# Kernel optimization log

Measured on AMD Instinct MI355X. Metric: run time of the kernel, lower is better.

The kernel has to match this reference:

```python
import jax, jax.numpy as jnp
import numpy as np

E, B, D, H, Z = 8, 16384, 512, 512, 64   # experts, batch, input_dim, hidden, latent
NHID = 2                                 # num_mlp_layers - 1 hidden-to-hidden layers


def setup_inputs() -> dict:
    key = jax.random.key(0)
    ks = jax.random.split(key, 12)

    def w(k, shape, fan_in):
        return (jax.random.normal(k, shape, jnp.float32) / np.sqrt(fan_in)).astype(jnp.float32)

    return {
        "x": jax.random.normal(ks[0], (B, D), jnp.float32),
        "eps": jax.random.normal(ks[1], (B, Z), jnp.float32),
        # stacked per-expert parameters (leading axis E)
        "enc_in_w": w(ks[2], (E, D, H), D), "enc_in_b": jnp.zeros((E, H), jnp.float32),
        "enc_hid_w": w(ks[3], (E, NHID, H, H), H), "enc_hid_b": jnp.zeros((E, NHID, H), jnp.float32),
        "mu_w": w(ks[4], (E, H, Z), H), "mu_b": jnp.zeros((E, Z), jnp.float32),
        "lv_w": w(ks[5], (E, H, Z), H), "lv_b": jnp.zeros((E, Z), jnp.float32),
        "dec_in_w": w(ks[6], (E, Z, H), Z), "dec_in_b": jnp.zeros((E, H), jnp.float32),
        "dec_hid_w": w(ks[7], (E, NHID, H, H), H), "dec_hid_b": jnp.zeros((E, NHID, H), jnp.float32),
        "dec_out_w": w(ks[8], (E, H, D), H), "dec_out_b": jnp.zeros((E, D), jnp.float32),
    }


def _moe_forward(x, eps, enc_in_w, enc_in_b, enc_hid_w, enc_hid_b,
                 mu_w, mu_b, lv_w, lv_b,
                 dec_in_w, dec_in_b, dec_hid_w, dec_hid_b, dec_out_w, dec_out_b):
    # ---- every expert tries the problem (dense, all experts over full batch) ----
    h = jax.nn.relu(jnp.einsum('bd,edh->ebh', x, enc_in_w) + enc_in_b[:, None, :])
    for i in range(NHID):
        h = jax.nn.relu(jnp.einsum('ebh,ehk->ebk', h, enc_hid_w[:, i]) + enc_hid_b[:, i, None, :])
    mu = jnp.einsum('ebh,ehz->ebz', h, mu_w) + mu_b[:, None, :]          # [E,B,Z]
    logvar = jnp.einsum('ebh,ehz->ebz', h, lv_w) + lv_b[:, None, :]       # [E,B,Z]
    z = mu + jnp.exp(0.5 * logvar) * eps[None, :, :]                      # reparameterize
    g = jax.nn.relu(jnp.einsum('ebz,ezh->ebh', z, dec_in_w) + dec_in_b[:, None, :])
    for i in range(NHID):
        g = jax.nn.relu(jnp.einsum('ebh,ehk->ebk', g, dec_hid_w[:, i]) + dec_hid_b[:, i, None, :])
    xhat = jnp.einsum('ebh,ehd->ebd', g, dec_out_w) + dec_out_b[:, None, :]  # [E,B,D]

    # ---- per-sample recon loss, pick best expert (torch.min over experts) ----
    recon = jnp.mean((xhat - x[None, :, :]) ** 2, axis=-1)                # [E,B]
    expert_idx = jnp.argmin(recon, axis=0)                                # [B]

    # ---- sparse_others: single fused gather instead of python loop ----
    bi = jnp.arange(x.shape[0])
    return mu[expert_idx, bi], logvar[expert_idx, bi], xhat[expert_idx, bi]


def reference(x, eps, enc_in_w, enc_in_b, enc_hid_w, enc_hid_b,
              mu_w, mu_b, lv_w, lv_b,
              dec_in_w, dec_in_b, dec_hid_w, dec_hid_b, dec_out_w, dec_out_b):
    return _moe_forward(x, eps, enc_in_w, enc_in_b, enc_hid_w, enc_hid_b,
                        mu_w, mu_b, lv_w, lv_b,
                        dec_in_w, dec_in_b, dec_hid_w, dec_hid_b, dec_out_w, dec_out_b)
```

## Files before the change

### kernel.cpp

```cpp
#include <hip/hip_runtime.h>
#include <cstdint>

#define Eexp 8
#define Bb   16384
#define Dd   512
#define Hh   512
#define Zz   64

typedef _Float16 f16x8 __attribute__((ext_vector_type(8)));
typedef float    f32x4 __attribute__((ext_vector_type(4)));

#define OFF_ENCIN  0
#define OFF_HID0   524288
#define OFF_HID1   1048576
#define OFF_HEADS  1572864
#define OFF_DECIN  1703936
#define OFF_DHID0  1769472
#define OFF_DHID1  2293760
#define OFF_DECOUT 2818048
#define PEREXP     3342336
#define WT_TOTAL   (8 * (size_t)PEREXP)

#define GLL16(g, l) __builtin_amdgcn_global_load_lds( \
    (const __attribute__((address_space(1))) void*)(g), \
    (__attribute__((address_space(3))) void*)(l), 16, 0, 0)

template<bool TR>
__global__ __launch_bounds__(256)
void fmsplit(const float* __restrict__ src, _Float16* __restrict__ dst,
             int KTOT, int inner, long sStride, long dStride)
{
    __shared__ float t[64][65];
    const int e  = blockIdx.z;
    const int o0 = blockIdx.x * 64;
    const int k0 = blockIdx.y * 64;
    const float* S = src + (size_t)e * sStride;
    _Float16*    D = dst + (size_t)e * dStride;
    const int tid = threadIdx.x;
    const int rr = tid >> 4, c4 = (tid & 15) * 4;
    #pragma unroll
    for (int p = 0; p < 4; ++p) {
        const int r = rr + p * 16;
        const float4 v = *reinterpret_cast<const float4*>(
            S + (size_t)(TR ? (k0 + r) : (o0 + r)) * inner + (TR ? o0 : k0) + c4);
        t[r][c4 + 0] = v.x; t[r][c4 + 1] = v.y;
        t[r][c4 + 2] = v.z; t[r][c4 + 3] = v.w;
    }
    __syncthreads();
    const int lane = tid & 63, wid = tid >> 6;
    const int KB = KTOT >> 5;
    #pragma unroll
    for (int p = 0; p < 2; ++p) {
        const int g  = wid * 2 + p;
        const int ot = g >> 1, kb = g & 1;
        const int rI = ot * 16 + (lane & 15);
        const int kI = kb * 32 + (lane >> 4) * 8;
        f16x8 hv, lv;
        #pragma unroll
        for (int j = 0; j < 8; ++j) {
            const float v = TR ? t[kI + j][rI] : t[rI][kI + j];
            const _Float16 h = (_Float16)v;
            hv[j] = h; lv[j] = (_Float16)(v - (float)h);
        }
        const size_t base = ((size_t)((o0 >> 4) + ot) * KB + (k0 >> 5) + kb) * 1024;
        *reinterpret_cast<f16x8*>(D + base + lane * 8)       = hv;
        *reinterpret_cast<f16x8*>(D + base + 512 + lane * 8) = lv;
    }
}

template<int KA>
__global__ __launch_bounds__(256, 2)
void gemm_mid(const _Float16* __restrict__ Afm, const _Float16* __restrict__ Wfm,
              const float* __restrict__ bias0, _Float16* __restrict__ Cfm)
{
    constexpr int KB  = KA / 32;
    constexpr int NT  = KB;
    constexpr int ACH = 16;
    constexpr int NCH = 32;
    constexpr int GPW = 8;
    __shared__ __align__(16) _Float16 lds[2 * NCH * 512];

    const int bid = blockIdx.x;
    const int bx = (bid & 7) * 16 + (bid >> 5);
    const int by = (bid >> 3) & 3;

    const int lane = threadIdx.x & 63, wid = threadIdx.x >> 6;
    const int wr = wid >> 1, wc = wid & 1;
    const int row0 = bx * 128;
    const int col0 = by * 128;

    const _Float16* src[GPW];
    #pragma unroll
    for (int p = 0; p < GPW; ++p) {
        const int q = wid * GPW + p;
        if (q < ACH)
            src[p] = Afm + (size_t)((row0 >> 4) + (q >> 1)) * KB * 1024
                         + (q & 1) * 512 + lane * 8;
        else {
            const int qq = q - ACH;
            src[p] = Wfm + (size_t)((col0 >> 4) + (qq >> 1)) * KB * 1024
                         + (qq & 1) * 512 + lane * 8;
        }
    }

    f32x4 acc[4][4];
    #pragma unroll
    for (int i = 0; i < 4; ++i)
        #pragma unroll
        for (int j = 0; j < 4; ++j) acc[i][j] = {0.f, 0.f, 0.f, 0.f};

#define STAGE(buf)                                                           \
    { _Pragma("unroll")                                                      \
      for (int p = 0; p < GPW; ++p) {                                        \
          GLL16(src[p], lds + (buf) * (NCH * 512) + (wid * GPW + p) * 512);  \
          src[p] += 1024;                                                    \
      } }

    STAGE(0)
    if (NT > 1) STAGE(1)

    for (int t = 0; t < NT; ++t) {
        if (t + 1 < NT) { asm volatile("s_waitcnt vmcnt(%0)" :: "i"(GPW) : "memory"); }
        else            { asm volatile("s_waitcnt vmcnt(0)" ::: "memory"); }
        __builtin_amdgcn_s_barrier();
        asm volatile("" ::: "memory");

        const _Float16* B0 = lds + (t & 1) * (NCH * 512);
        f16x8 ah[4], al[4], wh[4], wl[4];
        #pragma unroll
        for (int mf = 0; mf < 4; ++mf) {
            const int q = (wr * 4 + mf) * 2;
            ah[mf] = *reinterpret_cast<const f16x8*>(B0 + q * 512 + lane * 8);
            al[mf] = *reinterpret_cast<const f16x8*>(B0 + q * 512 + 512 + lane * 8);
        }
        #pragma unroll
        for (int nf = 0; nf < 4; ++nf) {
            const int q = ACH + (wc * 4 + nf) * 2;
            wh[nf] = *reinterpret_cast<const f16x8*>(B0 + q * 512 + lane * 8);
            wl[nf] = *reinterpret_cast<const f16x8*>(B0 + q * 512 + 512 + lane * 8);
        }
        __builtin_amdgcn_s_setprio(1);
        #pragma unroll
        for (int mf = 0; mf < 4; ++mf)
            #pragma unroll
            for (int nf = 0; nf < 4; ++nf) {
                acc[mf][nf] = __builtin_amdgcn_mfma_f32_16x16x32_f16(
                    ah[mf], wh[nf], acc[mf][nf], 0, 0, 0);
                acc[mf][nf] = __builtin_amdgcn_mfma_f32_16x16x32_f16(
                    ah[mf], wl[nf], acc[mf][nf], 0, 0, 0);
                acc[mf][nf] = __builtin_amdgcn_mfma_f32_16x16x32_f16(
                    al[mf], wh[nf], acc[mf][nf], 0, 0, 0);
            }
        __builtin_amdgcn_s_setprio(0);
        asm volatile("" ::: "memory");
        __builtin_amdgcn_s_barrier();
        asm volatile("" ::: "memory");
        if (t + 2 < NT) STAGE(t & 1)
    }
#undef STAGE

    uint32_t* sb = reinterpret_cast<uint32_t*>(&lds[0]);
    #pragma unroll
    for (int ph = 0; ph < 2; ++ph) {
        if (wc == ph) {
            #pragma unroll
            for (int nf = 0; nf < 4; ++nf) {
                const int c_l = nf * 16 + (lane & 15);
                const float bv = bias0[col0 + ph * 64 + c_l];
                #pragma unroll
                for (int mf = 0; mf < 4; ++mf)
                    #pragma unroll
                    for (int j = 0; j < 4; ++j) {
                        const int r_l = wr * 64 + mf * 16 + (lane >> 4) * 4 + j;
                        const float v = fmaxf(acc[mf][nf][j] + bv, 0.f);
                        const _Float16 h = (_Float16)v;
                        const _Float16 lo = (_Float16)(v - (float)h);
                        const uint32_t pk =
                            (uint32_t)__builtin_bit_cast(uint16_t, h) |
                            ((uint32_t)__builtin_bit_cast(uint16_t, lo) << 16);
                        sb[r_l * 64 + (((c_l >> 2) ^ (r_l & 15)) << 2) + (c_l & 3)] = pk;
                    }
            }
        }
        __syncthreads();
        {
            #pragma unroll
            for (int i = 0; i < 4; ++i) {
                const int q = wid * 4 + i;
                const int T_l = q >> 1, kb_l = q & 1;
                const int r_l = T_l * 16 + (lane & 15);
                const int cb  = kb_l * 32 + (lane >> 4) * 8;
                uint32_t u[8];
                #pragma unroll
                for (int jb = 0; jb < 2; ++jb) {
                    const int chunk = ((cb >> 2) + jb) ^ (r_l & 15);
                    const uint32_t* pp = &sb[r_l * 64 + chunk * 4];
                    u[jb*4+0] = pp[0]; u[jb*4+1] = pp[1];
                    u[jb*4+2] = pp[2]; u[jb*4+3] = pp[3];
                }
                f16x8 hv, lvv;
                #pragma unroll
                for (int j = 0; j < 8; ++j) {
                    hv[j]  = __builtin_bit_cast(_Float16, (uint16_t)(u[j] & 0xffff));
                    lvv[j] = __builtin_bit_cast(_Float16, (uint16_t)(u[j] >> 16));
                }
                const size_t base =
                    ((size_t)((row0 >> 4) + T_l) * 16 +
                     ((col0 + ph * 64) >> 5) + kb_l) * 1024;
                *reinterpret_cast<f16x8*>(Cfm + base + lane * 8)       = hv;
                *reinterpret_cast<f16x8*>(Cfm + base + 512 + lane * 8) = lvv;
            }
        }
        __syncthreads();
    }
}

__global__ __launch_bounds__(256, 2)
void heads_z(const _Float16* __restrict__ Afm, const _Float16* __restrict__ Wfm,
             const float* __restrict__ mu_b, const float* __restrict__ lv_b,
             const float* __restrict__ eps,
             float* __restrict__ mu_e, float* __restrict__ lv_e,
             _Float16* __restrict__ zfm)
{
    constexpr int KB = 16, NT = 16, ACH = 8, NCH = 24, GPW = 6;
    __shared__ __align__(16) _Float16 lds[2 * NCH * 512];

    const int bid = blockIdx.x;
    const int bx = (bid & 7) * 32 + (bid >> 3);
    const int lane = threadIdx.x & 63, wid = threadIdx.x >> 6;
    const int wr = wid >> 1, wc = wid & 1;
    const int row0 = bx * 64;

    const _Float16* src[GPW];
    #pragma unroll
    for (int p = 0; p < GPW; ++p) {
        const int q = wid * GPW + p;
        if (q < ACH)
            src[p] = Afm + (size_t)((row0 >> 4) + (q >> 1)) * KB * 1024
                         + (q & 1) * 512 + lane * 8;
        else {
            const int qq = q - ACH;
            src[p] = Wfm + (size_t)(qq >> 1) * KB * 1024 + (qq & 1) * 512 + lane * 8;
        }
    }

    f32x4 acc[2][4];
    #pragma unroll
    for (int i = 0; i < 2; ++i)
        #pragma unroll
        for (int j = 0; j < 4; ++j) acc[i][j] = {0.f, 0.f, 0.f, 0.f};

#define STAGE(buf)                                                           \
    { _Pragma("unroll")                                                      \
      for (int p = 0; p < GPW; ++p) {                                        \
          GLL16(src[p], lds + (buf) * (NCH * 512) + (wid * GPW + p) * 512);  \
          src[p] += 1024;                                                    \
      } }

    STAGE(0)
    STAGE(1)

    for (int t = 0; t < NT; ++t) {
        if (t + 1 < NT) { asm volatile("s_waitcnt vmcnt(%0)" :: "i"(GPW) : "memory"); }
        else            { asm volatile("s_waitcnt vmcnt(0)" ::: "memory"); }
        __builtin_amdgcn_s_barrier();
        asm volatile("" ::: "memory");

        const _Float16* B0 = lds + (t & 1) * (NCH * 512);
        f16x8 ah[2], al[2], wh[4], wl[4];
        #pragma unroll
        for (int mf = 0; mf < 2; ++mf) {
            const int q = (wr * 2 + mf) * 2;
            ah[mf] = *reinterpret_cast<const f16x8*>(B0 + q * 512 + lane * 8);
            al[mf] = *reinterpret_cast<const f16x8*>(B0 + q * 512 + 512 + lane * 8);
        }
        #pragma unroll
        for (int nf = 0; nf < 4; ++nf) {
            const int q = ACH + (wc * 4 + nf) * 2;
            wh[nf] = *reinterpret_cast<const f16x8*>(B0 + q * 512 + lane * 8);
            wl[nf] = *reinterpret_cast<const f16x8*>(B0 + q * 512 + 512 + lane * 8);
        }
        __builtin_amdgcn_s_setprio(1);
        #pragma unroll
        for (int mf = 0; mf < 2; ++mf)
            #pragma unroll
            for (int nf = 0; nf < 4; ++nf) {
                acc[mf][nf] = __builtin_amdgcn_mfma_f32_16x16x32_f16(
                    ah[mf], wh[nf], acc[mf][nf], 0, 0, 0);
                acc[mf][nf] = __builtin_amdgcn_mfma_f32_16x16x32_f16(
                    ah[mf], wl[nf], acc[mf][nf], 0, 0, 0);
                acc[mf][nf] = __builtin_amdgcn_mfma_f32_16x16x32_f16(
                    al[mf], wh[nf], acc[mf][nf], 0, 0, 0);
            }
        __builtin_amdgcn_s_setprio(0);
        asm volatile("" ::: "memory");
        __builtin_amdgcn_s_barrier();
        asm volatile("" ::: "memory");
        if (t + 2 < NT) STAGE(t & 1)
    }
#undef STAGE

    float* mulv = reinterpret_cast<float*>(&lds[0]);
    #pragma unroll
    for (int nf = 0; nf < 4; ++nf) {
        const int c_h = wc * 64 + nf * 16 + (lane & 15);
        const float bv = (c_h < 64) ? mu_b[c_h] : lv_b[c_h - 64];
        #pragma unroll
        for (int mf = 0; mf < 2; ++mf)
            #pragma unroll
            for (int j = 0; j < 4; ++j) {
                const int r_l = wr * 32 + mf * 16 + (lane >> 4) * 4 + j;
                mulv[r_l * 128 + c_h] = acc[mf][nf][j] + bv;
            }
    }
    __syncthreads();
    const int tid = threadIdx.x;
    #pragma unroll
    for (int k = 0; k < 16; ++k) {
        const int id  = tid + k * 256;
        const int r_l = id >> 6, c = id & 63;
        const float m = mulv[r_l * 128 + c];
        const float l = mulv[r_l * 128 + 64 + c];
        const size_t go = (size_t)(row0 + r_l) * 64 + c;
        const float ev = eps[go];
        const float z  = m + expf(0.5f * l) * ev;
        mu_e[go] = m; lv_e[go] = l;
        const _Float16 h  = (_Float16)z;
        const _Float16 lo = (_Float16)(z - (float)h);
        const size_t base = ((size_t)((row0 + r_l) >> 4) * 2 + (c >> 5)) * 1024
                            + ((r_l & 15) + ((c >> 3) & 3) * 16) * 8 + (c & 7);
        zfm[base]       = h;
        zfm[base + 512] = lo;
    }
}

__global__ __launch_bounds__(512, 2)
void dec_out_fused(const _Float16* __restrict__ Afm, const _Float16* __restrict__ Wfm,
                   const float* __restrict__ bias,
                   const float* __restrict__ Xin,
                   const float* __restrict__ mu_e, const float* __restrict__ lv_e,
                   float* __restrict__ best,
                   float* __restrict__ out_mu, float* __restrict__ out_lv,
                   float* __restrict__ out_xh, int isFirst)
{
    constexpr int KB = 16, NT = 16, ACH = 8, NCH = 72, GPW = 9;
    __shared__ __align__(16) _Float16 lds[2 * NCH * 512];

    const int bid = blockIdx.x;
    const int bx = (bid & 7) * 32 + (bid >> 3);
    const int lane = threadIdx.x & 63, wid = threadIdx.x >> 6;
    const int row0 = bx * 64;
    const int colW = wid * 64;

    const _Float16* src[GPW];
    #pragma unroll
    for (int p = 0; p < GPW; ++p) {
        const int q = wid * GPW + p;
        if (q < ACH)
            src[p] = Afm + (size_t)((row0 >> 4) + (q >> 1)) * KB * 1024
                         + (q & 1) * 512 + lane * 8;
        else {
            const int qq = q - ACH;
            src[p] = Wfm + (size_t)(qq >> 1) * KB * 1024 + (qq & 1) * 512 + lane * 8;
        }
    }

    f32x4 acc[4][4];
    #pragma unroll
    for (int i = 0; i < 4; ++i)
        #pragma unroll
        for (int j = 0; j < 4; ++j) acc[i][j] = {0.f, 0.f, 0.f, 0.f};

#define STAGE(buf)                                                           \
    { _Pragma("unroll")                                                      \
      for (int p = 0; p < GPW; ++p) {                                        \
          GLL16(src[p], lds + (buf) * (NCH * 512) + (wid * GPW + p) * 512);  \
          src[p] += 1024;                                                    \
      } }

    STAGE(0)
    STAGE(1)

    for (int t = 0; t < NT; ++t) {
        if (t + 1 < NT) { asm volatile("s_waitcnt vmcnt(%0)" :: "i"(GPW) : "memory"); }
        else            { asm volatile("s_waitcnt vmcnt(0)" ::: "memory"); }
        __builtin_amdgcn_s_barrier();
        asm volatile("" ::: "memory");

        const _Float16* B0 = lds + (t & 1) * (NCH * 512);
        f16x8 ah[4], al[4], wh[4], wl[4];
        #pragma unroll
        for (int mf = 0; mf < 4; ++mf) {
            const int q = mf * 2;
            ah[mf] = *reinterpret_cast<const f16x8*>(B0 + q * 512 + lane * 8);
            al[mf] = *reinterpret_cast<const f16x8*>(B0 + q * 512 + 512 + lane * 8);
        }
        #pragma unroll
        for (int nf = 0; nf < 4; ++nf) {
            const int q = ACH + (wid * 4 + nf) * 2;
            wh[nf] = *reinterpret_cast<const f16x8*>(B0 + q * 512 + lane * 8);
            wl[nf] = *reinterpret_cast<const f16x8*>(B0 + q * 512 + 512 + lane * 8);
        }
        __builtin_amdgcn_s_setprio(1);
        #pragma unroll
        for (int mf = 0; mf < 4; ++mf)
            #pragma unroll
            for (int nf = 0; nf < 4; ++nf) {
                acc[mf][nf] = __builtin_amdgcn_mfma_f32_16x16x32_f16(
                    ah[mf], wh[nf], acc[mf][nf], 0, 0, 0);
                acc[mf][nf] = __builtin_amdgcn_mfma_f32_16x16x32_f16(
                    ah[mf], wl[nf], acc[mf][nf], 0, 0, 0);
                acc[mf][nf] = __builtin_amdgcn_mfma_f32_16x16x32_f16(
                    al[mf], wh[nf], acc[mf][nf], 0, 0, 0);
            }
        __builtin_amdgcn_s_setprio(0);
        asm volatile("" ::: "memory");
        __builtin_amdgcn_s_barrier();
        asm volatile("" ::: "memory");
        if (t + 2 < NT) STAGE(t & 1)
    }
#undef STAGE

    float*    recP = reinterpret_cast<float*>(&lds[0]);
    int*      winf = reinterpret_cast<int*>(recP + 8 * 64);

    float rsum[4][4];
    #pragma unroll
    for (int mf = 0; mf < 4; ++mf)
        #pragma unroll
        for (int j = 0; j < 4; ++j) rsum[mf][j] = 0.f;
    float bv[4];
    #pragma unroll
    for (int nf = 0; nf < 4; ++nf) bv[nf] = bias[colW + nf * 16 + (lane & 15)];
    #pragma unroll
    for (int nf = 0; nf < 4; ++nf) {
        const int col = colW + nf * 16 + (lane & 15);
        #pragma unroll
        for (int mf = 0; mf < 4; ++mf)
            #pragma unroll
            for (int j = 0; j < 4; ++j) {
                const int r_l = mf * 16 + (lane >> 4) * 4 + j;
                const float v = acc[mf][nf][j] + bv[nf];
                const float d = v - Xin[(size_t)(row0 + r_l) * 512 + col];
                rsum[mf][j] += d * d;
            }
    }
    #pragma unroll
    for (int mf = 0; mf < 4; ++mf)
        #pragma unroll
        for (int j = 0; j < 4; ++j) {
            float s = rsum[mf][j];
            s += __shfl_xor(s, 1); s += __shfl_xor(s, 2);
            s += __shfl_xor(s, 4); s += __shfl_xor(s, 8);
            if ((lane & 15) == 0)
                recP[wid * 64 + mf * 16 + (lane >> 4) * 4 + j] = s;
        }
    __syncthreads();
    if (wid == 0) {
        float r = 0.f;
        #pragma unroll
        for (int w = 0; w < 8; ++w) r += recP[w * 64 + lane];
        const int grow = row0 + lane;
        const bool w = isFirst || (r < best[grow]);
        if (w) best[grow] = r;
        winf[lane] = w ? 1 : 0;
    }
    __syncthreads();
    #pragma unroll
    for (int mf = 0; mf < 4; ++mf)
        #pragma unroll
        for (int j = 0; j < 4; ++j) {
            const int r_l = mf * 16 + (lane >> 4) * 4 + j;
            if (winf[r_l]) {
                #pragma unroll
                for (int nf = 0; nf < 4; ++nf) {
                    const int col = colW + nf * 16 + (lane & 15);
                    out_xh[(size_t)(row0 + r_l) * 512 + col] = acc[mf][nf][j] + bv[nf];
                }
            }
        }
    if (wid == 0) {
        for (int r = 0; r < 64; ++r)
            if (winf[r]) {
                const size_t o = (size_t)(row0 + r) * 64 + lane;
                out_mu[o] = mu_e[o];
            }
    } else if (wid == 1) {
        for (int r = 0; r < 64; ++r)
            if (winf[r]) {
                const size_t o = (size_t)(row0 + r) * 64 + lane;
                out_lv[o] = lv_e[o];
            }
    }
}

extern "C" void kernel_launch(void* const* d_in, const int* in_sizes, int n_in,
                              void* d_out, int out_size, void* d_ws, size_t ws_size,
                              hipStream_t stream)
{
    const float* x         = (const float*)d_in[0];
    const float* eps       = (const float*)d_in[1];
    const float* enc_in_w  = (const float*)d_in[2];
    const float* enc_in_b  = (const float*)d_in[3];
    const float* enc_hid_w = (const float*)d_in[4];
    const float* enc_hid_b = (const float*)d_in[5];
    const float* mu_w      = (const float*)d_in[6];
    const float* mu_b      = (const float*)d_in[7];
    const float* lv_w      = (const float*)d_in[8];
    const float* lv_b      = (const float*)d_in[9];
    const float* dec_in_w  = (const float*)d_in[10];
    const float* dec_in_b  = (const float*)d_in[11];
    const float* dec_hid_w = (const float*)d_in[12];
    const float* dec_hid_b = (const float*)d_in[13];
    const float* dec_out_w = (const float*)d_in[14];
    const float* dec_out_b = (const float*)d_in[15];

    const size_t FM = (size_t)Bb * 512 * 2;
    const size_t BZ = (size_t)Bb * 64;

    _Float16* wt  = (_Float16*)d_ws;
    _Float16* xfm = wt + WT_TOTAL;
    _Float16* afm = xfm + FM;
    _Float16* bfm = afm + FM;
    _Float16* zfm = bfm + FM;
    float* fbase  = (float*)(zfm + (size_t)Bb * 64 * 2);
    float* mu_e   = fbase;
    float* lv_e   = mu_e + BZ;
    float* best   = lv_e + BZ;

    float* out_mu = (float*)d_out;
    float* out_lv = out_mu + (size_t)Bb * Zz;
    float* out_xh = out_lv + (size_t)Bb * Zz;

    const dim3 blk(256);

    fmsplit<true ><<<dim3(8, 8, 8), blk, 0, stream>>>(enc_in_w,           wt + OFF_ENCIN,  512, 512, 262144, PEREXP);
    fmsplit<true ><<<dim3(8, 8, 8), blk, 0, stream>>>(enc_hid_w,          wt + OFF_HID0,   512, 512, 524288, PEREXP);
    fmsplit<true ><<<dim3(8, 8, 8), blk, 0, stream>>>(enc_hid_w + 262144, wt + OFF_HID1,   512, 512, 524288, PEREXP);
    fmsplit<true ><<<dim3(1, 8, 8), blk, 0, stream>>>(mu_w,               wt + OFF_HEADS,  512,  64,  32768, PEREXP);
    fmsplit<true ><<<dim3(1, 8, 8), blk, 0, stream>>>(lv_w,        wt + OFF_HEADS + 65536, 512,  64,  32768, PEREXP);
    fmsplit<true ><<<dim3(8, 1, 8), blk, 0, stream>>>(dec_in_w,           wt + OFF_DECIN,   64, 512,  32768, PEREXP);
    fmsplit<true ><<<dim3(8, 8, 8), blk, 0, stream>>>(dec_hid_w,          wt + OFF_DHID0,  512, 512, 524288, PEREXP);
    fmsplit<true ><<<dim3(8, 8, 8), blk, 0, stream>>>(dec_hid_w + 262144, wt + OFF_DHID1,  512, 512, 524288, PEREXP);
    fmsplit<true ><<<dim3(8, 8, 8), blk, 0, stream>>>(dec_out_w,          wt + OFF_DECOUT, 512, 512, 262144, PEREXP);
    fmsplit<false><<<dim3(256, 8, 1), blk, 0, stream>>>(x,                xfm,             512, 512, 0, 0);

    const dim3 g512(512), g256(256), blk512(512);

    for (int e = 0; e < Eexp; ++e) {
        const _Float16* we = wt + (size_t)e * PEREXP;
        gemm_mid<512><<<g512, blk, 0, stream>>>(
            xfm, we + OFF_ENCIN, enc_in_b + (size_t)e * Hh, afm);
        gemm_mid<512><<<g512, blk, 0, stream>>>(
            afm, we + OFF_HID0, enc_hid_b + ((size_t)e * 2 + 0) * Hh, bfm);
        gemm_mid<512><<<g512, blk, 0, stream>>>(
            bfm, we + OFF_HID1, enc_hid_b + ((size_t)e * 2 + 1) * Hh, afm);
        heads_z<<<g256, blk, 0, stream>>>(
            afm, we + OFF_HEADS, mu_b + (size_t)e * Zz, lv_b + (size_t)e * Zz,
            eps, mu_e, lv_e, zfm);
        gemm_mid< 64><<<g512, blk, 0, stream>>>(
            zfm, we + OFF_DECIN, dec_in_b + (size_t)e * Hh, bfm);
        gemm_mid<512><<<g512, blk, 0, stream>>>(
            bfm, we + OFF_DHID0, dec_hid_b + ((size_t)e * 2 + 0) * Hh, afm);
        gemm_mid<512><<<g512, blk, 0, stream>>>(
            afm, we + OFF_DHID1, dec_hid_b + ((size_t)e * 2 + 1) * Hh, bfm);
        dec_out_fused<<<g256, blk512, 0, stream>>>(
            bfm, we + OFF_DECOUT, dec_out_b + (size_t)e * Dd,
            x, mu_e, lv_e, best, out_mu, out_lv, out_xh, e == 0 ? 1 : 0);
    }
}
```

Baseline: 1.757 ms.

## Load decoder-output weights straight to registers and shrink LDS staging to activations

The dec_out_fused kernel now stages only the activation tiles through LDS with async global-to-LDS loads. Each wave reads its own weight fragments directly from global memory into registers every k-step, instead of staging all 72 chunks through LDS. LDS usage drops sharply and launch bounds change to one block per SIMD hint, which allows more registers. The mu/logvar winner copy is also spread across all 8 waves instead of 2. The risks are exposed global-load latency on the weight reads, since they are issued just before the wait, and a fragile hand-tuned vmcnt accounting.

```diff
diff --git a/kernel.cpp b/kernel.cpp
--- a/kernel.cpp
+++ b/kernel.cpp
@@ -334,7 +334,7 @@
     }
 }
 
-__global__ __launch_bounds__(512, 2)
+__global__ __launch_bounds__(512, 1)
 void dec_out_fused(const _Float16* __restrict__ Afm, const _Float16* __restrict__ Wfm,
                    const float* __restrict__ bias,
                    const float* __restrict__ Xin,
@@ -343,8 +343,8 @@
                    float* __restrict__ out_mu, float* __restrict__ out_lv,
                    float* __restrict__ out_xh, int isFirst)
 {
-    constexpr int KB = 16, NT = 16, ACH = 8, NCH = 72, GPW = 9;
-    __shared__ __align__(16) _Float16 lds[2 * NCH * 512];
+    constexpr int KB = 16, NT = 16;
+    __shared__ __align__(16) _Float16 lds[2 * 8 * 512];
 
     const int bid = blockIdx.x;
     const int bx = (bid & 7) * 32 + (bid >> 3);
@@ -352,18 +352,13 @@
     const int row0 = bx * 64;
     const int colW = wid * 64;
 
-    const _Float16* src[GPW];
-    #pragma unroll
-    for (int p = 0; p < GPW; ++p) {
-        const int q = wid * GPW + p;
-        if (q < ACH)
-            src[p] = Afm + (size_t)((row0 >> 4) + (q >> 1)) * KB * 1024
-                         + (q & 1) * 512 + lane * 8;
-        else {
-            const int qq = q - ACH;
-            src[p] = Wfm + (size_t)(qq >> 1) * KB * 1024 + (qq & 1) * 512 + lane * 8;
-        }
-    }
+    const _Float16* aSrc = Afm + (size_t)((row0 >> 4) + (wid >> 1)) * KB * 1024
+                               + (wid & 1) * 512 + lane * 8;
+    const _Float16* wSrc[8];
+    #pragma unroll
+    for (int i = 0; i < 8; ++i)
+        wSrc[i] = Wfm + (size_t)(wid * 4 + (i >> 1)) * KB * 1024
+                      + (i & 1) * 512 + lane * 8;
 
     f32x4 acc[4][4];
     #pragma unroll
@@ -371,35 +366,32 @@
         #pragma unroll
         for (int j = 0; j < 4; ++j) acc[i][j] = {0.f, 0.f, 0.f, 0.f};
 
-#define STAGE(buf)                                                           \
-    { _Pragma("unroll")                                                      \
-      for (int p = 0; p < GPW; ++p) {                                        \
-          GLL16(src[p], lds + (buf) * (NCH * 512) + (wid * GPW + p) * 512);  \
-          src[p] += 1024;                                                    \
-      } }
-
-    STAGE(0)
-    STAGE(1)
+#define STAGE_A(buf)                                                         \
+    { GLL16(aSrc, lds + (buf) * 4096 + wid * 512); aSrc += 1024; }
+
+    STAGE_A(0)
+    STAGE_A(1)
 
     for (int t = 0; t < NT; ++t) {
-        if (t + 1 < NT) { asm volatile("s_waitcnt vmcnt(%0)" :: "i"(GPW) : "memory"); }
-        else            { asm volatile("s_waitcnt vmcnt(0)" ::: "memory"); }
+        f16x8 wh[4], wl[4];
+        #pragma unroll
+        for (int nf = 0; nf < 4; ++nf) {
+            wh[nf] = *reinterpret_cast<const f16x8*>(wSrc[nf * 2]);
+            wl[nf] = *reinterpret_cast<const f16x8*>(wSrc[nf * 2 + 1]);
+            wSrc[nf * 2]     += 1024;
+            wSrc[nf * 2 + 1] += 1024;
+        }
+        if (t + 1 < NT) { asm volatile("s_waitcnt vmcnt(9)" ::: "memory"); }
+        else            { asm volatile("s_waitcnt vmcnt(8)" ::: "memory"); }
         __builtin_amdgcn_s_barrier();
         asm volatile("" ::: "memory");
 
-        const _Float16* B0 = lds + (t & 1) * (NCH * 512);
-        f16x8 ah[4], al[4], wh[4], wl[4];
+        const _Float16* B0 = lds + (t & 1) * 4096;
+        f16x8 ah[4], al[4];
         #pragma unroll
         for (int mf = 0; mf < 4; ++mf) {
-            const int q = mf * 2;
-            ah[mf] = *reinterpret_cast<const f16x8*>(B0 + q * 512 + lane * 8);
-            al[mf] = *reinterpret_cast<const f16x8*>(B0 + q * 512 + 512 + lane * 8);
-        }
-        #pragma unroll
-        for (int nf = 0; nf < 4; ++nf) {
-            const int q = ACH + (wid * 4 + nf) * 2;
-            wh[nf] = *reinterpret_cast<const f16x8*>(B0 + q * 512 + lane * 8);
-            wl[nf] = *reinterpret_cast<const f16x8*>(B0 + q * 512 + 512 + lane * 8);
+            ah[mf] = *reinterpret_cast<const f16x8*>(B0 + mf * 1024 + lane * 8);
+            al[mf] = *reinterpret_cast<const f16x8*>(B0 + mf * 1024 + 512 + lane * 8);
         }
         __builtin_amdgcn_s_setprio(1);
         #pragma unroll
@@ -417,12 +409,12 @@
         asm volatile("" ::: "memory");
         __builtin_amdgcn_s_barrier();
         asm volatile("" ::: "memory");
-        if (t + 2 < NT) STAGE(t & 1)
-    }
-#undef STAGE
-
-    float*    recP = reinterpret_cast<float*>(&lds[0]);
-    int*      winf = reinterpret_cast<int*>(recP + 8 * 64);
+        if (t + 2 < NT) STAGE_A(t & 1)
+    }
+#undef STAGE_A
+
+    float* recP = reinterpret_cast<float*>(&lds[0]);
+    int*   winf = reinterpret_cast<int*>(recP + 8 * 64);
 
     float rsum[4][4];
     #pragma unroll
@@ -479,18 +471,14 @@
                 }
             }
         }
-    if (wid == 0) {
-        for (int r = 0; r < 64; ++r)
-            if (winf[r]) {
-                const size_t o = (size_t)(row0 + r) * 64 + lane;
-                out_mu[o] = mu_e[o];
-            }
-    } else if (wid == 1) {
-        for (int r = 0; r < 64; ++r)
-            if (winf[r]) {
-                const size_t o = (size_t)(row0 + r) * 64 + lane;
-                out_lv[o] = lv_e[o];
-            }
+    #pragma unroll
+    for (int k = 0; k < 8; ++k) {
+        const int r = wid * 8 + k;
+        if (winf[r]) {
+            const size_t o = (size_t)(row0 + r) * 64 + lane;
+            out_mu[o] = mu_e[o];
+            out_lv[o] = lv_e[o];
+        }
     }
 }
 
```

After: 1.683 ms. -4.2%, faster.
